# Kernel optimization log

Measured on AMD Instinct MI355X. Metric: run time of the kernel, lower is better.

## Reference

```python
import jax, jax.numpy as jnp
from jax import lax
import numpy as np

T, B, D, H = 4096, 32, 512, 256


def setup_inputs() -> dict:
    key = jax.random.key(0)
    ks = jax.random.split(key, 8)
    s_ih = 1.0 / np.sqrt(H)
    inp = {
        "x": jax.random.normal(ks[0], (T, B, D), dtype=jnp.float32),
        "reset": jax.random.randint(ks[1], (T, B), 0, 2, dtype=jnp.int32),
        # PyTorch nn.LSTM params, gate order (i, f, g, o)
        "W_ih": jax.random.uniform(ks[2], (4 * H, D), jnp.float32, -s_ih, s_ih),
        "W_hh": jax.random.uniform(ks[3], (4 * H, H), jnp.float32, -s_ih, s_ih),
        "b_ih": jax.random.uniform(ks[4], (4 * H,), jnp.float32, -s_ih, s_ih),
        "b_hh": jax.random.uniform(ks[5], (4 * H,), jnp.float32, -s_ih, s_ih),
        "W_proj": jax.random.uniform(ks[6], (1, H), jnp.float32, -s_ih, s_ih),
        "b_proj": jax.random.uniform(ks[7], (1,), jnp.float32, -s_ih, s_ih),
    }
    return inp


def _lstm_with_reset(x, reset, W_ih, W_hh, b_ih, b_hh):
    # Precompute input contribution for all timesteps: [T, B, 4H]
    xW = jnp.einsum("tbd,gd->tbg", x, W_ih) + b_ih + b_hh
    h0 = jnp.zeros((x.shape[1], H), x.dtype)
    c0 = jnp.zeros((x.shape[1], H), x.dtype)

    def step(carry, inp):
        h, c = carry
        xw, r = inp
        keep = (1 - r).astype(h.dtype)[:, None]  # zero state at episode starts
        h = h * keep
        c = c * keep
        gates = xw + h @ W_hh.T  # [B, 4H]
        i, f, g, o = jnp.split(gates, 4, axis=-1)
        c = jax.nn.sigmoid(f) * c + jax.nn.sigmoid(i) * jnp.tanh(g)
        h = jax.nn.sigmoid(o) * jnp.tanh(c)
        return (h, c), h

    (_, _), hs = lax.scan(step, (h0, c0), (xW, reset))
    return hs  # [T, B, H]


def reference(x, reset, W_ih, W_hh, b_ih, b_hh, W_proj, b_proj):
    hs = _lstm_with_reset(x, reset, W_ih, W_hh, b_ih, b_hh)
    return hs @ W_proj.T + b_proj  # [T, B, 1]
```

## Files before the change

### kernel.cpp

```cpp
#include <hip/hip_runtime.h>
#include <cstdint>
#include <cstddef>

#define T_DIM 4096
#define B_DIM 32
#define D_DIM 512
#define H_DIM 256
#define G_DIM 1024
#define HSTR 264
#define XSTR 1036
#define NBUCK 64

typedef _Float16 h8 __attribute__((ext_vector_type(8)));
typedef float f4 __attribute__((ext_vector_type(4)));

__global__ void seg_build_kernel(const int* __restrict__ reset,
                                 unsigned* __restrict__ starts,
                                 unsigned* __restrict__ segcnt) {
  __shared__ unsigned cnts[256];
  __shared__ unsigned offs[256];
  const int b = blockIdx.x;
  const int tid = threadIdx.x;
  const int t0 = tid * 16;
  unsigned c = 0;
  for (int e = 0; e < 16; ++e) {
    int t = t0 + e;
    bool pred = (t == 0) || (reset[t * B_DIM + b] != 0);
    c += pred ? 1u : 0u;
  }
  cnts[tid] = c;
  __syncthreads();
  if (tid == 0) {
    unsigned run = 0;
    for (int i = 0; i < 256; ++i) { unsigned v = cnts[i]; offs[i] = run; run += v; }
    segcnt[b] = run;
  }
  __syncthreads();
  unsigned o = (unsigned)b * 4096u + offs[tid];
  for (int e = 0; e < 16; ++e) {
    int t = t0 + e;
    bool pred = (t == 0) || (reset[t * B_DIM + b] != 0);
    if (pred) { starts[o++] = (unsigned)t; }
  }
}

__global__ void seg_flat_kernel(const unsigned* __restrict__ starts,
                                const unsigned* __restrict__ segcnt,
                                uint2* __restrict__ flat2,
                                unsigned* __restrict__ meta) {
  __shared__ unsigned offs;
  const int b = blockIdx.x;
  const int tid = threadIdx.x;
  if (tid == 0) {
    unsigned o = 0;
    for (int i = 0; i < b; ++i) o += segcnt[i];
    offs = o;
    if (b == 31) meta[1] = o + segcnt[31];
    if (b == 0) meta[0] = 0u;
  }
  __syncthreads();
  const unsigned cnt = segcnt[b];
  const unsigned off = offs;
  for (unsigned s = tid; s < cnt; s += 256) {
    unsigned t0 = starts[b * 4096u + s];
    unsigned t1 = (s + 1 < cnt) ? starts[b * 4096u + s + 1] : 4096u;
    flat2[off + s] = make_uint2(t0 | ((unsigned)b << 16), t1);
  }
}

__global__ void seg_sort_kernel(const uint2* __restrict__ flat2,
                                uint2* __restrict__ flat,
                                const unsigned* __restrict__ meta) {
  __shared__ unsigned lh[NBUCK];
  __shared__ unsigned cur[NBUCK];
  const unsigned nseg = meta[1];
  const int tid = threadIdx.x;
  const int lane = tid & 63;
  if (tid < NBUCK) lh[tid] = 0u;
  __syncthreads();
  for (unsigned base = 0; base < nseg; base += 1024) {
    unsigned i = base + tid;
    bool act = i < nseg;
    unsigned bk = 0u;
    if (act) {
      uint2 e = flat2[i];
      bk = min(e.y - (e.x & 0xFFFFu), (unsigned)NBUCK) - 1u;
    }
    unsigned long long rem = __ballot(act);
    while (rem) {
      int ld = (int)__ffsll((unsigned long long)rem) - 1;
      unsigned lbk = __shfl(bk, ld);
      unsigned long long meq = __ballot(act && bk == lbk);
      if (lane == ld) atomicAdd(&lh[lbk], (unsigned)__popcll(meq));
      rem &= ~meq;
    }
  }
  __syncthreads();
  if (tid == 0) {
    unsigned run = 0;
    for (int k = NBUCK - 1; k >= 0; --k) { cur[k] = run; run += lh[k]; }
  }
  __syncthreads();
  for (unsigned base = 0; base < nseg; base += 1024) {
    unsigned i = base + tid;
    bool act = i < nseg;
    uint2 e = make_uint2(0u, 0u);
    unsigned bk = 0u;
    if (act) {
      e = flat2[i];
      bk = min(e.y - (e.x & 0xFFFFu), (unsigned)NBUCK) - 1u;
    }
    unsigned long long rem = __ballot(act);
    unsigned pos = 0u;
    while (rem) {
      int ld = (int)__ffsll((unsigned long long)rem) - 1;
      unsigned lbk = __shfl(bk, ld);
      unsigned long long meq = __ballot(act && bk == lbk);
      unsigned bs = 0u;
      if (lane == ld) bs = atomicAdd(&cur[lbk], (unsigned)__popcll(meq));
      bs = __shfl(bs, ld);
      if (act && bk == lbk)
        pos = bs + (unsigned)__popcll(meq & ((1ull << lane) - 1ull));
      rem &= ~meq;
    }
    if (act) flat[pos] = e;
  }
}

__global__ void wpack_kernel(const float* __restrict__ Whh,
                             _Float16* __restrict__ wpack) {
  int gid = blockIdx.x * 256 + threadIdx.x;
  int nt = gid >> 9;
  int rem = gid & 511;
  int ks = rem >> 6;
  int l = rem & 63;
  int n = nt * 16 + (l & 15);
  int k = ks * 32 + (l >> 4) * 8;
  const float* src = Whh + (size_t)n * H_DIM + k;
  f4 v0 = *(const f4*)src;
  f4 v1 = *(const f4*)(src + 4);
  h8 wv = {(_Float16)v0.x, (_Float16)v0.y, (_Float16)v0.z, (_Float16)v0.w,
           (_Float16)v1.x, (_Float16)v1.y, (_Float16)v1.z, (_Float16)v1.w};
  *(h8*)(wpack + (size_t)gid * 8) = wv;
}

__global__ __launch_bounds__(256) void xcvt_kernel(const float* __restrict__ X,
                                                   _Float16* __restrict__ xh) {
  const int n8 = (T_DIM * B_DIM * D_DIM) / 8;
  int stride = gridDim.x * blockDim.x;
  for (int i = blockIdx.x * blockDim.x + threadIdx.x; i < n8; i += stride) {
    const float* s = X + (size_t)i * 8;
    f4 a = *(const f4*)s;
    f4 b = *(const f4*)(s + 4);
    h8 v = {(_Float16)a.x, (_Float16)a.y, (_Float16)a.z, (_Float16)a.w,
            (_Float16)b.x, (_Float16)b.y, (_Float16)b.z, (_Float16)b.w};
    *(h8*)(xh + (size_t)i * 8) = v;
  }
}

__global__ void wihpack_kernel(const float* __restrict__ Wih,
                               _Float16* __restrict__ wihp) {
  int gid = blockIdx.x * 256 + threadIdx.x;
  int nt = gid >> 10;
  int ks = (gid >> 6) & 15;
  int l = gid & 63;
  int n = nt * 16 + (l & 15);
  int k = ks * 32 + (l >> 4) * 8;
  const float* src = Wih + (size_t)n * D_DIM + k;
  f4 v0 = *(const f4*)src;
  f4 v1 = *(const f4*)(src + 4);
  h8 wv = {(_Float16)v0.x, (_Float16)v0.y, (_Float16)v0.z, (_Float16)v0.w,
           (_Float16)v1.x, (_Float16)v1.y, (_Float16)v1.z, (_Float16)v1.w};
  *(h8*)(wihp + (size_t)gid * 8) = wv;
}

#define BM 128
#define BN 128
#define BK 32

__global__ __launch_bounds__(256) void xw_gemm_direct(
    const _Float16* __restrict__ xh, const _Float16* __restrict__ wihp,
    const float* __restrict__ bih, const float* __restrict__ bhh,
    _Float16* __restrict__ xw) {
  const int tid = threadIdx.x;
  const int lane = tid & 63;
  const int wave = tid >> 6;
  const unsigned wg = blockIdx.x;
  const unsigned xcd = wg & 7u;
  const unsigned idx = wg >> 3;
  const size_t m0 = (size_t)(xcd * 128u + (idx >> 3)) * BM;
  const int n0 = (int)(idx & 7u) * BN;
  const int wm = (wave & 1) * 64;
  const int wn = (wave >> 1) * 64;
  const int q = lane >> 4;
  const int r = lane & 15;

  f4 acc[4][4];
#pragma unroll
  for (int i = 0; i < 4; ++i)
#pragma unroll
    for (int j = 0; j < 4; ++j) { f4 z = {0.f, 0.f, 0.f, 0.f}; acc[i][j] = z; }

  const _Float16* aBase = xh + (m0 + (size_t)(wm + r)) * D_DIM + q * 8;
  const _Float16* bBase = wihp + ((size_t)(((n0 + wn) >> 4) * 16) * 64 + lane) * 8;

#pragma unroll 4
  for (int ks = 0; ks < 16; ++ks) {
    h8 af[4], bf[4];
#pragma unroll
    for (int mi = 0; mi < 4; ++mi)
      af[mi] = *(const h8*)(aBase + (size_t)mi * (16 * D_DIM) + ks * 32);
#pragma unroll
    for (int ni = 0; ni < 4; ++ni)
      bf[ni] = *(const h8*)(bBase + (size_t)(ni * 16 + ks) * (64 * 8));
#pragma unroll
    for (int mi = 0; mi < 4; ++mi)
#pragma unroll
      for (int ni = 0; ni < 4; ++ni)
        acc[mi][ni] = __builtin_amdgcn_mfma_f32_16x16x32_f16(af[mi], bf[ni], acc[mi][ni], 0, 0, 0);
  }

#pragma unroll
  for (int mi = 0; mi < 4; ++mi) {
#pragma unroll
    for (int ni = 0; ni < 4; ++ni) {
      int n = n0 + wn + ni * 16 + r;
      float bias = bih[n] + bhh[n];
#pragma unroll
      for (int reg = 0; reg < 4; ++reg) {
        size_t m = m0 + (size_t)(wm + mi * 16 + q * 4 + reg);
        xw[m * G_DIM + n] = (_Float16)(acc[mi][ni][reg] + bias);
      }
    }
  }
}

__global__ __launch_bounds__(256) void xw_gemm_kernel(
    const float* __restrict__ X, const float* __restrict__ Wih,
    const float* __restrict__ bih, const float* __restrict__ bhh,
    _Float16* __restrict__ xw) {
  __shared__ _Float16 As[BM * BK];
  __shared__ _Float16 Bs[BN * BK];
  const int tid = threadIdx.x;
  const int lane = tid & 63;
  const int wave = tid >> 6;
  const unsigned wg = blockIdx.x;
  const unsigned xcd = wg & 7u;
  const unsigned idx = wg >> 3;
  const size_t m0 = (size_t)(xcd * 128u + (idx >> 3)) * BM;
  const int n0 = (int)(idx & 7u) * BN;
  const int wm = (wave & 1) * 64;
  const int wn = (wave >> 1) * 64;
  const int q = lane >> 4;
  const int r = lane & 15;

  f4 acc[4][4];
#pragma unroll
  for (int i = 0; i < 4; ++i)
#pragma unroll
    for (int j = 0; j < 4; ++j) { f4 z = {0.f, 0.f, 0.f, 0.f}; acc[i][j] = z; }

  const int srow = tid >> 1;
  const int kh = (tid & 1) * 16;

  for (int k0 = 0; k0 < D_DIM; k0 += BK) {
    const float* ax = X + (m0 + (size_t)srow) * D_DIM + k0 + kh;
    const float* bx = Wih + ((size_t)(n0 + srow)) * D_DIM + k0 + kh;
    f4 a0 = *(const f4*)(ax);
    f4 a1 = *(const f4*)(ax + 4);
    f4 a2 = *(const f4*)(ax + 8);
    f4 a3 = *(const f4*)(ax + 12);
    f4 b0 = *(const f4*)(bx);
    f4 b1 = *(const f4*)(bx + 4);
    f4 b2 = *(const f4*)(bx + 8);
    f4 b3 = *(const f4*)(bx + 12);
    h8 ha0 = {(_Float16)a0.x, (_Float16)a0.y, (_Float16)a0.z, (_Float16)a0.w,
              (_Float16)a1.x, (_Float16)a1.y, (_Float16)a1.z, (_Float16)a1.w};
    h8 ha1 = {(_Float16)a2.x, (_Float16)a2.y, (_Float16)a2.z, (_Float16)a2.w,
              (_Float16)a3.x, (_Float16)a3.y, (_Float16)a3.z, (_Float16)a3.w};
    h8 hb0 = {(_Float16)b0.x, (_Float16)b0.y, (_Float16)b0.z, (_Float16)b0.w,
              (_Float16)b1.x, (_Float16)b1.y, (_Float16)b1.z, (_Float16)b1.w};
    h8 hb1 = {(_Float16)b2.x, (_Float16)b2.y, (_Float16)b2.z, (_Float16)b2.w,
              (_Float16)b3.x, (_Float16)b3.y, (_Float16)b3.z, (_Float16)b3.w};
    *(h8*)(As + srow * BK + kh) = ha0;
    *(h8*)(As + srow * BK + kh + 8) = ha1;
    *(h8*)(Bs + srow * BK + kh) = hb0;
    *(h8*)(Bs + srow * BK + kh + 8) = hb1;
    __syncthreads();

    h8 af[4], bf[4];
#pragma unroll
    for (int mi = 0; mi < 4; ++mi)
      af[mi] = *(const h8*)(As + (wm + mi * 16 + r) * BK + q * 8);
#pragma unroll
    for (int ni = 0; ni < 4; ++ni)
      bf[ni] = *(const h8*)(Bs + (wn + ni * 16 + r) * BK + q * 8);
#pragma unroll
    for (int mi = 0; mi < 4; ++mi)
#pragma unroll
      for (int ni = 0; ni < 4; ++ni)
        acc[mi][ni] = __builtin_amdgcn_mfma_f32_16x16x32_f16(af[mi], bf[ni], acc[mi][ni], 0, 0, 0);
    __syncthreads();
  }

#pragma unroll
  for (int mi = 0; mi < 4; ++mi) {
#pragma unroll
    for (int ni = 0; ni < 4; ++ni) {
      int n = n0 + wn + ni * 16 + r;
      float bias = bih[n] + bhh[n];
#pragma unroll
      for (int reg = 0; reg < 4; ++reg) {
        size_t m = m0 + (size_t)(wm + mi * 16 + q * 4 + reg);
        xw[m * G_DIM + n] = (_Float16)(acc[mi][ni][reg] + bias);
      }
    }
  }
}

__device__ __forceinline__ float sigmf(float x) {
  return __builtin_amdgcn_rcpf(1.f + __expf(-x));
}
__device__ __forceinline__ float tanhf_(float x) {
  return 2.f * __builtin_amdgcn_rcpf(1.f + __expf(-2.f * x)) - 1.f;
}
__device__ __forceinline__ f4 MF(h8 a, h8 b, f4 c) {
  return __builtin_amdgcn_mfma_f32_16x16x32_f16(a, b, c, 0, 0, 0);
}

#define WPKp(g, j, ks) \
  ((const h8*)(wpack + (((size_t)((((g)*16 + 2*w + (j)) * 8 + (ks))) * 64 + l) * 8)))
#define ARD(mt, ks) (*(const h8*)(Hbuf + (16*(mt) + r16) * HSTR + (ks)*32 + q*8))

#define MFK_REG(KS) do {                                                   \
  h8 a0_ = ARD(0, KS), a1_ = ARD(1, KS);                                   \
  _Pragma("unroll") for (int g = 0; g < 4; ++g)                            \
  _Pragma("unroll") for (int j = 0; j < 2; ++j) {                          \
    acc[0][g][j] = MF(a0_, wr[g][j][KS], acc[0][g][j]);                    \
    acc[1][g][j] = MF(a1_, wr[g][j][KS], acc[1][g][j]); }                  \
} while (0)

#define MFK_W2() do {                                                      \
  h8 a0_ = ARD(0, 2), a1_ = ARD(1, 2);                                     \
  _Pragma("unroll") for (int g = 0; g < 4; ++g)                            \
  _Pragma("unroll") for (int j = 0; j < 2; ++j) {                          \
    h8 b_ = *(const h8*)(Wlds + (size_t)((((g)*16 + 2*w + (j)) * 64 + l)) * 8); \
    acc[0][g][j] = MF(a0_, b_, acc[0][g][j]);                              \
    acc[1][g][j] = MF(a1_, b_, acc[1][g][j]); }                            \
} while (0)

#define MFK_S(BUF, KS) do {                                                \
  h8 a0_ = ARD(0, KS), a1_ = ARD(1, KS);                                   \
  _Pragma("unroll") for (int g = 0; g < 4; ++g)                            \
  _Pragma("unroll") for (int j = 0; j < 2; ++j) {                          \
    acc[0][g][j] = MF(a0_, BUF[g][j], acc[0][g][j]);                       \
    acc[1][g][j] = MF(a1_, BUF[g][j], acc[1][g][j]); }                     \
} while (0)

#define LOAD_S(BUF, KS) do {                                               \
  _Pragma("unroll") for (int g = 0; g < 4; ++g)                            \
  _Pragma("unroll") for (int j = 0; j < 2; ++j)                            \
    BUF[g][j] = *WPKp(g, j, KS);                                           \
} while (0)

#define XRD(MT, G, J) do {                                                 \
  f4 xv;                                                                   \
  int rb_ = 16*(MT) + q*4;                                                 \
  int nn_ = (G)*256 + w*32 + 16*(J) + r16;                                 \
  xv.x = (float)xwlds[(rb_+0)*XSTR + nn_];                                 \
  xv.y = (float)xwlds[(rb_+1)*XSTR + nn_];                                 \
  xv.z = (float)xwlds[(rb_+2)*XSTR + nn_];                                 \
  xv.w = (float)xwlds[(rb_+3)*XSTR + nn_];                                 \
  acc[MT][G][J] += xv; } while (0)

#define CONTROL_STEP do {                                                     \
  int m = tid;                                                                \
  bool aliv = alivef[m] != 0;                                                 \
  if (aliv) {                                                                 \
    unsigned oi = outix[m];                                                   \
    if (oi != 0xFFFFFFFFu) {                                                  \
      float s = bp;                                                           \
      _Pragma("unroll") for (int ww = 0; ww < 8; ++ww) s += pbuf[ww][m];      \
      __builtin_nontemporal_store(s, &out[oi]);                               \
    }                                                                         \
  }                                                                           \
  bool cont = aliv && (tcur[m] + 1 < tend[m]);                                \
  bool need = aliv && !cont;                                                  \
  unsigned long long bal = __ballot(need);                                    \
  if (cont) {                                                                 \
    int t = tcur[m] + 1;                                                      \
    tcur[m] = t; keepm[m] = 1.f;                                              \
    unsigned row = (unsigned)t * 32u + (unsigned)bcol[m];                     \
    trowB[m] = row * 2048u; outix[m] = row;                                   \
  }                                                                           \
  if (bal) {                                                                  \
    unsigned cntp = (unsigned)__popcll(bal);                                  \
    int ldr = (int)__ffsll(bal) - 1;                                          \
    unsigned basep = 0;                                                       \
    if ((tid & 63) == ldr) basep = atomicAdd(ctr, cntp);                      \
    basep = __shfl(basep, ldr);                                               \
    if (need) {                                                               \
      unsigned idx = basep +                                                  \
          (unsigned)__popcll(bal & ((1ull << (tid & 63)) - 1ull));            \
      if (idx < nseg) {                                                       \
        uint2 sg = flat[idx];                                                 \
        int t0s = (int)(sg.x & 0xFFFFu); int bb = (int)(sg.x >> 16);          \
        tcur[m] = t0s; tend[m] = (int)sg.y; bcol[m] = bb; keepm[m] = 0.f;     \
        unsigned row = (unsigned)t0s * 32u + (unsigned)bb;                    \
        trowB[m] = row * 2048u; outix[m] = row;                               \
        h8 zz = {0,0,0,0,0,0,0,0};                                            \
        _Pragma("unroll") for (int i2 = 0; i2 < 33; ++i2)                     \
          *(h8*)(Hbuf + (size_t)m * HSTR + i2 * 8) = zz;                      \
      } else {                                                                \
        alivef[m] = 0; outix[m] = 0xFFFFFFFFu; trowB[m] = 0;                  \
        keepm[m] = 0.f;                                                       \
      }                                                                       \
    }                                                                         \
  }                                                                           \
} while (0)

__global__ __attribute__((amdgpu_flat_work_group_size(512, 512),
                          amdgpu_waves_per_eu(2, 2)))
void lstm_scan_mfma(
    const _Float16* __restrict__ xw,
    const _Float16* __restrict__ wpack,
    const float* __restrict__ Wproj,
    const float* __restrict__ bproj,
    const uint2* __restrict__ flat,
    unsigned* __restrict__ meta,
    float* __restrict__ out) {
  __shared__ __align__(16) _Float16 Wlds[64 * 64 * 8];
  __shared__ __align__(16) _Float16 xwlds[32 * XSTR];
  __shared__ __align__(16) _Float16 Hbuf[32 * HSTR];
  __shared__ __align__(16) float pbuf[8][32];
  __shared__ __align__(16) unsigned trowB[32];
  __shared__ __align__(16) float keepm[32];
  __shared__ unsigned outix[32];
  __shared__ int tcur[32], tend[32], bcol[32], alivef[32];

  const int tid = threadIdx.x;
  const int l = tid & 63;
  const int w = tid >> 6;
  const int q = l >> 4;
  const int r16 = l & 15;
  const char* xwc = (const char*)xw;
  unsigned* ctr = meta;
  const unsigned nseg = meta[1];

  for (int it = 0; it < 16; ++it) {
    int idx = it * 512 + tid;
    int nt = idx >> 6;
    int ll = idx & 63;
    *(h8*)(Wlds + (size_t)idx * 8) =
        *(const h8*)(wpack + (((size_t)(nt * 8 + 2)) * 64 + ll) * 8);
  }
  for (int i = tid; i < 32 * HSTR / 8; i += 512) {
    h8 z = {0,0,0,0,0,0,0,0};
    *(h8*)(Hbuf + (size_t)i * 8) = z;
  }
  h8 wr[4][2][2];
#pragma unroll
  for (int g = 0; g < 4; ++g)
#pragma unroll
    for (int j = 0; j < 2; ++j)
#pragma unroll
      for (int ks = 0; ks < 2; ++ks)
        wr[g][j][ks] = *WPKp(g, j, ks);

  const float wpv0 = Wproj[32 * w + r16];
  const float wpv1 = Wproj[32 * w + 16 + r16];
  const float bp = bproj[0];
  if (tid < 32) {
    alivef[tid] = 1; tcur[tid] = 0; tend[tid] = 0; bcol[tid] = 0;
    outix[tid] = 0xFFFFFFFFu; trowB[tid] = 0; keepm[tid] = 0.f;
  }
  float cst[16];
#pragma unroll
  for (int i = 0; i < 16; ++i) cst[i] = 0.f;
  __syncthreads();
  if (tid < 32) CONTROL_STEP;
  int nalive = __syncthreads_count(tid < 32 ? alivef[tid] : 0);

  while (nalive > 0) {
#pragma unroll
    for (int rnd = 0; rnd < 8; ++rnd) {
      int c = rnd * 8 + w;
      unsigned rowB = trowB[c >> 1];
      const char* src = xwc + (size_t)rowB + (size_t)((c & 1) * 1024) + (size_t)l * 16;
      _Float16* dst = xwlds + (size_t)(c >> 1) * XSTR + (c & 1) * 512;
      __builtin_amdgcn_global_load_lds((const uint32_t*)src, (uint32_t*)dst, 16, 0, 2);
    }

    f4 z4 = {0.f, 0.f, 0.f, 0.f};
    f4 acc[2][4][2];
#pragma unroll
    for (int mt = 0; mt < 2; ++mt)
#pragma unroll
      for (int g = 0; g < 4; ++g)
#pragma unroll
        for (int j = 0; j < 2; ++j) acc[mt][g][j] = z4;
    h8 sA[4][2], sB[4][2];

    LOAD_S(sA, 3); LOAD_S(sB, 4);
    MFK_REG(0);
    MFK_REG(1);
    MFK_W2();
    MFK_S(sA, 3); LOAD_S(sA, 5);
    MFK_S(sB, 4); LOAD_S(sB, 6);
    MFK_S(sA, 5); LOAD_S(sA, 7);
    MFK_S(sB, 6);
    MFK_S(sA, 7);

    __syncthreads();

    XRD(0, 0, 0); XRD(0, 0, 1);
    XRD(0, 1, 0); XRD(0, 1, 1);
    XRD(0, 2, 0); XRD(0, 2, 1);
    XRD(0, 3, 0); XRD(0, 3, 1);
    XRD(1, 0, 0); XRD(1, 0, 1);
    XRD(1, 1, 0); XRD(1, 1, 1);
    XRD(1, 2, 0); XRD(1, 2, 1);
    XRD(1, 3, 0); XRD(1, 3, 1);

    f4 kp0 = *(const f4*)&keepm[q * 4];
    f4 kp1 = *(const f4*)&keepm[16 + q * 4];
    float pr[8];
#pragma unroll
    for (int r = 0; r < 4; ++r) {
      {
        float gi = sigmf(acc[0][0][0][r]);
        float gf = sigmf(acc[0][1][0][r]);
        float gg = tanhf_(acc[0][2][0][r]);
        float go = sigmf(acc[0][3][0][r]);
        float cn = gf * (cst[r] * kp0[r]) + gi * gg;
        cst[r] = cn;
        float hv = go * tanhf_(cn);
        Hbuf[(q * 4 + r) * HSTR + 32 * w + r16] = (_Float16)hv;
        pr[r] = hv * wpv0;
      }
      {
        float gi = sigmf(acc[0][0][1][r]);
        float gf = sigmf(acc[0][1][1][r]);
        float gg = tanhf_(acc[0][2][1][r]);
        float go = sigmf(acc[0][3][1][r]);
        float cn = gf * (cst[4 + r] * kp0[r]) + gi * gg;
        cst[4 + r] = cn;
        float hv = go * tanhf_(cn);
        Hbuf[(q * 4 + r) * HSTR + 32 * w + 16 + r16] = (_Float16)hv;
        pr[r] += hv * wpv1;
      }
    }
#pragma unroll
    for (int r = 0; r < 4; ++r) {
      {
        float gi = sigmf(acc[1][0][0][r]);
        float gf = sigmf(acc[1][1][0][r]);
        float gg = tanhf_(acc[1][2][0][r]);
        float go = sigmf(acc[1][3][0][r]);
        float cn = gf * (cst[8 + r] * kp1[r]) + gi * gg;
        cst[8 + r] = cn;
        float hv = go * tanhf_(cn);
        Hbuf[(16 + q * 4 + r) * HSTR + 32 * w + r16] = (_Float16)hv;
        pr[4 + r] = hv * wpv0;
      }
      {
        float gi = sigmf(acc[1][0][1][r]);
        float gf = sigmf(acc[1][1][1][r]);
        float gg = tanhf_(acc[1][2][1][r]);
        float go = sigmf(acc[1][3][1][r]);
        float cn = gf * (cst[12 + r] * kp1[r]) + gi * gg;
        cst[12 + r] = cn;
        float hv = go * tanhf_(cn);
        Hbuf[(16 + q * 4 + r) * HSTR + 32 * w + 16 + r16] = (_Float16)hv;
        pr[4 + r] += hv * wpv1;
      }
    }
#pragma unroll
    for (int jj = 0; jj < 8; ++jj) {
      pr[jj] += __shfl_xor(pr[jj], 1);
      pr[jj] += __shfl_xor(pr[jj], 2);
      pr[jj] += __shfl_xor(pr[jj], 4);
      pr[jj] += __shfl_xor(pr[jj], 8);
    }
    if (r16 == 0) {
#pragma unroll
      for (int jj = 0; jj < 8; ++jj)
        pbuf[w][16 * (jj >> 2) + q * 4 + (jj & 3)] = pr[jj];
    }

    __syncthreads();
    if (tid < 32) CONTROL_STEP;
    nalive = __syncthreads_count(tid < 32 ? alivef[tid] : 0);
  }
}

extern "C" void kernel_launch(void* const* d_in, const int* in_sizes, int n_in,
                              void* d_out, int out_size, void* d_ws, size_t ws_size,
                              hipStream_t stream) {
  const float* x = (const float*)d_in[0];
  const int* reset = (const int*)d_in[1];
  const float* Wih = (const float*)d_in[2];
  const float* Whh = (const float*)d_in[3];
  const float* bih = (const float*)d_in[4];
  const float* bhh = (const float*)d_in[5];
  const float* Wproj = (const float*)d_in[6];
  const float* bproj = (const float*)d_in[7];
  float* out = (float*)d_out;

  char* ws = (char*)d_ws;
  _Float16* xw = (_Float16*)ws;
  unsigned* starts = (unsigned*)(ws + 268435456ULL);
  unsigned* segcnt = (unsigned*)(ws + 268959744ULL);
  uint2* flat = (uint2*)(ws + 268959872ULL);
  _Float16* wpack = (_Float16*)(ws + 270008448ULL);
  unsigned* meta = (unsigned*)(ws + 270532736ULL);
  _Float16* xh = (_Float16*)(ws + 270532864ULL);
  _Float16* wihp = (_Float16*)(ws + 404750592ULL);
  const bool big = ws_size >= 405799168ULL;
  uint2* flat2 = (uint2*)ws;

  hipLaunchKernelGGL(seg_build_kernel, dim3(32), dim3(256), 0, stream,
                     reset, starts, segcnt);
  hipLaunchKernelGGL(seg_flat_kernel, dim3(32), dim3(256), 0, stream,
                     starts, segcnt, flat2, meta);
  hipLaunchKernelGGL(seg_sort_kernel, dim3(1), dim3(1024), 0, stream,
                     flat2, flat, meta);
  hipLaunchKernelGGL(wpack_kernel, dim3(128), dim3(256), 0, stream,
                     Whh, wpack);
  if (big) {
    hipLaunchKernelGGL(xcvt_kernel, dim3(2048), dim3(256), 0, stream, x, xh);
    hipLaunchKernelGGL(wihpack_kernel, dim3(256), dim3(256), 0, stream,
                       Wih, wihp);
    hipLaunchKernelGGL(xw_gemm_direct, dim3(8192), dim3(256), 0, stream,
                       xh, wihp, bih, bhh, xw);
  } else {
    hipLaunchKernelGGL(xw_gemm_kernel, dim3(8192), dim3(256), 0, stream,
                       x, Wih, bih, bhh, xw);
  }
  hipLaunchKernelGGL(lstm_scan_mfma, dim3(256), dim3(512), 0, stream,
                     xw, wpack, Wproj, bproj, flat, meta, out);
}
```

Baseline: 1.318 ms.

## Use LDS-staged f16 GEMM for input projection and 16-wave LSTM scan blocks

Replaces the direct-from-global packed-weight input GEMM with an LDS-staged version. It converts W_ih to plain row-major f16 and fills shared memory with global_load_lds in K=64 chunks. The recurrent scan kernel now runs 1024 threads (16 waves) per block instead of 512, so each wave owns 16 hidden columns rather than 32. This halves per-thread accumulators, register-held W_hh fragments and cell state, aiming to spread the per-step recurrent GEMM and gate math over more waves. The cost is more waves meeting at each per-step barrier, a larger projection reduction, and a global_load_lds cache-policy change.

```diff
diff --git a/kernel.cpp b/kernel.cpp
--- a/kernel.cpp
+++ b/kernel.cpp
@@ -158,38 +158,35 @@
   }
 }
 
-__global__ void wihpack_kernel(const float* __restrict__ Wih,
-                               _Float16* __restrict__ wihp) {
-  int gid = blockIdx.x * 256 + threadIdx.x;
-  int nt = gid >> 10;
-  int ks = (gid >> 6) & 15;
-  int l = gid & 63;
-  int n = nt * 16 + (l & 15);
-  int k = ks * 32 + (l >> 4) * 8;
-  const float* src = Wih + (size_t)n * D_DIM + k;
-  f4 v0 = *(const f4*)src;
-  f4 v1 = *(const f4*)(src + 4);
-  h8 wv = {(_Float16)v0.x, (_Float16)v0.y, (_Float16)v0.z, (_Float16)v0.w,
-           (_Float16)v1.x, (_Float16)v1.y, (_Float16)v1.z, (_Float16)v1.w};
-  *(h8*)(wihp + (size_t)gid * 8) = wv;
-}
-
-#define BM 128
-#define BN 128
-#define BK 32
-
-__global__ __launch_bounds__(256) void xw_gemm_direct(
-    const _Float16* __restrict__ xh, const _Float16* __restrict__ wihp,
+__global__ __launch_bounds__(256) void whcvt_kernel(const float* __restrict__ Wih,
+                                                    _Float16* __restrict__ whp) {
+  int i = blockIdx.x * 256 + threadIdx.x;
+  const float* s = Wih + (size_t)i * 8;
+  f4 a = *(const f4*)s;
+  f4 b = *(const f4*)(s + 4);
+  h8 v = {(_Float16)a.x, (_Float16)a.y, (_Float16)a.z, (_Float16)a.w,
+          (_Float16)b.x, (_Float16)b.y, (_Float16)b.z, (_Float16)b.w};
+  *(h8*)(whp + (size_t)i * 8) = v;
+}
+
+#define GBM 128
+#define GBN 128
+#define GBK 64
+
+__global__ __launch_bounds__(256) void xw_gemm_f16(
+    const _Float16* __restrict__ xh, const _Float16* __restrict__ whp,
     const float* __restrict__ bih, const float* __restrict__ bhh,
     _Float16* __restrict__ xw) {
+  __shared__ __align__(16) _Float16 As[GBM * GBK];
+  __shared__ __align__(16) _Float16 Bs[GBN * GBK];
   const int tid = threadIdx.x;
   const int lane = tid & 63;
   const int wave = tid >> 6;
   const unsigned wg = blockIdx.x;
   const unsigned xcd = wg & 7u;
   const unsigned idx = wg >> 3;
-  const size_t m0 = (size_t)(xcd * 128u + (idx >> 3)) * BM;
-  const int n0 = (int)(idx & 7u) * BN;
+  const size_t m0 = (size_t)(xcd * 128u + (idx >> 3)) * GBM;
+  const int n0 = (int)(idx & 7u) * GBN;
   const int wm = (wave & 1) * 64;
   const int wn = (wave >> 1) * 64;
   const int q = lane >> 4;
@@ -201,23 +198,44 @@
 #pragma unroll
     for (int j = 0; j < 4; ++j) { f4 z = {0.f, 0.f, 0.f, 0.f}; acc[i][j] = z; }
 
-  const _Float16* aBase = xh + (m0 + (size_t)(wm + r)) * D_DIM + q * 8;
-  const _Float16* bBase = wihp + ((size_t)(((n0 + wn) >> 4) * 16) * 64 + lane) * 8;
-
-#pragma unroll 4
-  for (int ks = 0; ks < 16; ++ks) {
-    h8 af[4], bf[4];
+  const char* aSrc = (const char*)xh + m0 * (D_DIM * 2);
+  const char* bSrc = (const char*)whp + (size_t)n0 * (D_DIM * 2);
+
+  for (int k0 = 0; k0 < D_DIM; k0 += GBK) {
+#pragma unroll
+    for (int i = 0; i < 4; ++i) {
+      int o = tid * 16 + i * 4096;
+      int row = o >> 7;
+      int colb = o & 127;
+      __builtin_amdgcn_global_load_lds(
+          (const uint32_t*)(aSrc + (size_t)row * (D_DIM * 2) + k0 * 2 + colb),
+          (uint32_t*)((char*)As + o), 16, 0, 0);
+      __builtin_amdgcn_global_load_lds(
+          (const uint32_t*)(bSrc + (size_t)row * (D_DIM * 2) + k0 * 2 + colb),
+          (uint32_t*)((char*)Bs + o), 16, 0, 0);
+    }
+    __syncthreads();
+
+    h8 af[4][2], bf[4][2];
 #pragma unroll
     for (int mi = 0; mi < 4; ++mi)
-      af[mi] = *(const h8*)(aBase + (size_t)mi * (16 * D_DIM) + ks * 32);
+#pragma unroll
+      for (int ks = 0; ks < 2; ++ks)
+        af[mi][ks] = *(const h8*)(As + (wm + mi * 16 + r) * GBK + ks * 32 + q * 8);
 #pragma unroll
     for (int ni = 0; ni < 4; ++ni)
-      bf[ni] = *(const h8*)(bBase + (size_t)(ni * 16 + ks) * (64 * 8));
-#pragma unroll
-    for (int mi = 0; mi < 4; ++mi)
-#pragma unroll
-      for (int ni = 0; ni < 4; ++ni)
-        acc[mi][ni] = __builtin_amdgcn_mfma_f32_16x16x32_f16(af[mi], bf[ni], acc[mi][ni], 0, 0, 0);
+#pragma unroll
+      for (int ks = 0; ks < 2; ++ks)
+        bf[ni][ks] = *(const h8*)(Bs + (wn + ni * 16 + r) * GBK + ks * 32 + q * 8);
+#pragma unroll
+    for (int ks = 0; ks < 2; ++ks)
+#pragma unroll
+      for (int mi = 0; mi < 4; ++mi)
+#pragma unroll
+        for (int ni = 0; ni < 4; ++ni)
+          acc[mi][ni] = __builtin_amdgcn_mfma_f32_16x16x32_f16(
+              af[mi][ks], bf[ni][ks], acc[mi][ni], 0, 0, 0);
+    __syncthreads();
   }
 
 #pragma unroll
@@ -234,6 +252,10 @@
     }
   }
 }
+
+#define BM 128
+#define BN 128
+#define BK 32
 
 __global__ __launch_bounds__(256) void xw_gemm_kernel(
     const float* __restrict__ X, const float* __restrict__ Wih,
@@ -328,50 +350,46 @@
   return __builtin_amdgcn_mfma_f32_16x16x32_f16(a, b, c, 0, 0, 0);
 }
 
-#define WPKp(g, j, ks) \
-  ((const h8*)(wpack + (((size_t)((((g)*16 + 2*w + (j)) * 8 + (ks))) * 64 + l) * 8)))
+#define WPK16(g, ks) \
+  ((const h8*)(wpack + (((size_t)(((g)*16 + w) * 8 + (ks))) * 64 + l) * 8))
 #define ARD(mt, ks) (*(const h8*)(Hbuf + (16*(mt) + r16) * HSTR + (ks)*32 + q*8))
 
 #define MFK_REG(KS) do {                                                   \
   h8 a0_ = ARD(0, KS), a1_ = ARD(1, KS);                                   \
-  _Pragma("unroll") for (int g = 0; g < 4; ++g)                            \
-  _Pragma("unroll") for (int j = 0; j < 2; ++j) {                          \
-    acc[0][g][j] = MF(a0_, wr[g][j][KS], acc[0][g][j]);                    \
-    acc[1][g][j] = MF(a1_, wr[g][j][KS], acc[1][g][j]); }                  \
+  _Pragma("unroll") for (int g = 0; g < 4; ++g) {                          \
+    acc[0][g] = MF(a0_, wr[g][KS], acc[0][g]);                             \
+    acc[1][g] = MF(a1_, wr[g][KS], acc[1][g]); }                           \
 } while (0)
 
 #define MFK_W2() do {                                                      \
   h8 a0_ = ARD(0, 2), a1_ = ARD(1, 2);                                     \
-  _Pragma("unroll") for (int g = 0; g < 4; ++g)                            \
-  _Pragma("unroll") for (int j = 0; j < 2; ++j) {                          \
-    h8 b_ = *(const h8*)(Wlds + (size_t)((((g)*16 + 2*w + (j)) * 64 + l)) * 8); \
-    acc[0][g][j] = MF(a0_, b_, acc[0][g][j]);                              \
-    acc[1][g][j] = MF(a1_, b_, acc[1][g][j]); }                            \
+  _Pragma("unroll") for (int g = 0; g < 4; ++g) {                          \
+    h8 b_ = *(const h8*)(Wlds + (size_t)((((g)*16 + w) * 64 + l)) * 8);    \
+    acc[0][g] = MF(a0_, b_, acc[0][g]);                                    \
+    acc[1][g] = MF(a1_, b_, acc[1][g]); }                                  \
 } while (0)
 
 #define MFK_S(BUF, KS) do {                                                \
   h8 a0_ = ARD(0, KS), a1_ = ARD(1, KS);                                   \
-  _Pragma("unroll") for (int g = 0; g < 4; ++g)                            \
-  _Pragma("unroll") for (int j = 0; j < 2; ++j) {                          \
-    acc[0][g][j] = MF(a0_, BUF[g][j], acc[0][g][j]);                       \
-    acc[1][g][j] = MF(a1_, BUF[g][j], acc[1][g][j]); }                     \
+  _Pragma("unroll") for (int g = 0; g < 4; ++g) {                          \
+    acc[0][g] = MF(a0_, BUF[g], acc[0][g]);                                \
+    acc[1][g] = MF(a1_, BUF[g], acc[1][g]); }                              \
 } while (0)
 
 #define LOAD_S(BUF, KS) do {                                               \
   _Pragma("unroll") for (int g = 0; g < 4; ++g)                            \
-  _Pragma("unroll") for (int j = 0; j < 2; ++j)                            \
-    BUF[g][j] = *WPKp(g, j, KS);                                           \
+    BUF[g] = *WPK16(g, KS);                                                \
 } while (0)
 
-#define XRD(MT, G, J) do {                                                 \
+#define XRD(MT, G) do {                                                    \
   f4 xv;                                                                   \
   int rb_ = 16*(MT) + q*4;                                                 \
-  int nn_ = (G)*256 + w*32 + 16*(J) + r16;                                 \
+  int nn_ = (G)*256 + hh;                                                  \
   xv.x = (float)xwlds[(rb_+0)*XSTR + nn_];                                 \
   xv.y = (float)xwlds[(rb_+1)*XSTR + nn_];                                 \
   xv.z = (float)xwlds[(rb_+2)*XSTR + nn_];                                 \
   xv.w = (float)xwlds[(rb_+3)*XSTR + nn_];                                 \
-  acc[MT][G][J] += xv; } while (0)
+  acc[MT][G] += xv; } while (0)
 
 #define CONTROL_STEP do {                                                     \
   int m = tid;                                                                \
@@ -380,7 +398,7 @@
     unsigned oi = outix[m];                                                   \
     if (oi != 0xFFFFFFFFu) {                                                  \
       float s = bp;                                                           \
-      _Pragma("unroll") for (int ww = 0; ww < 8; ++ww) s += pbuf[ww][m];      \
+      _Pragma("unroll") for (int ww = 0; ww < 16; ++ww) s += pbuf[ww][m];     \
       __builtin_nontemporal_store(s, &out[oi]);                               \
     }                                                                         \
   }                                                                           \
@@ -419,9 +437,7 @@
   }                                                                           \
 } while (0)
 
-__global__ __attribute__((amdgpu_flat_work_group_size(512, 512),
-                          amdgpu_waves_per_eu(2, 2)))
-void lstm_scan_mfma(
+__global__ __launch_bounds__(1024) void lstm_scan_mfma(
     const _Float16* __restrict__ xw,
     const _Float16* __restrict__ wpack,
     const float* __restrict__ Wproj,
@@ -432,7 +448,7 @@
   __shared__ __align__(16) _Float16 Wlds[64 * 64 * 8];
   __shared__ __align__(16) _Float16 xwlds[32 * XSTR];
   __shared__ __align__(16) _Float16 Hbuf[32 * HSTR];
-  __shared__ __align__(16) float pbuf[8][32];
+  __shared__ __align__(16) float pbuf[16][32];
   __shared__ __align__(16) unsigned trowB[32];
   __shared__ __align__(16) float keepm[32];
   __shared__ unsigned outix[32];
@@ -443,63 +459,57 @@
   const int w = tid >> 6;
   const int q = l >> 4;
   const int r16 = l & 15;
+  const int hh = 16 * w + r16;
   const char* xwc = (const char*)xw;
   unsigned* ctr = meta;
   const unsigned nseg = meta[1];
 
-  for (int it = 0; it < 16; ++it) {
-    int idx = it * 512 + tid;
+  for (int it = 0; it < 4; ++it) {
+    int idx = it * 1024 + tid;
     int nt = idx >> 6;
     int ll = idx & 63;
     *(h8*)(Wlds + (size_t)idx * 8) =
         *(const h8*)(wpack + (((size_t)(nt * 8 + 2)) * 64 + ll) * 8);
   }
-  for (int i = tid; i < 32 * HSTR / 8; i += 512) {
+  for (int i = tid; i < 32 * HSTR / 8; i += 1024) {
     h8 z = {0,0,0,0,0,0,0,0};
     *(h8*)(Hbuf + (size_t)i * 8) = z;
   }
-  h8 wr[4][2][2];
+  h8 wr[4][2];
 #pragma unroll
   for (int g = 0; g < 4; ++g)
 #pragma unroll
-    for (int j = 0; j < 2; ++j)
-#pragma unroll
-      for (int ks = 0; ks < 2; ++ks)
-        wr[g][j][ks] = *WPKp(g, j, ks);
-
-  const float wpv0 = Wproj[32 * w + r16];
-  const float wpv1 = Wproj[32 * w + 16 + r16];
+    for (int ks = 0; ks < 2; ++ks)
+      wr[g][ks] = *WPK16(g, ks);
+
+  const float wpv = Wproj[hh];
   const float bp = bproj[0];
   if (tid < 32) {
     alivef[tid] = 1; tcur[tid] = 0; tend[tid] = 0; bcol[tid] = 0;
     outix[tid] = 0xFFFFFFFFu; trowB[tid] = 0; keepm[tid] = 0.f;
   }
-  float cst[16];
-#pragma unroll
-  for (int i = 0; i < 16; ++i) cst[i] = 0.f;
+  float cst[8] = {0, 0, 0, 0, 0, 0, 0, 0};
   __syncthreads();
   if (tid < 32) CONTROL_STEP;
   int nalive = __syncthreads_count(tid < 32 ? alivef[tid] : 0);
 
   while (nalive > 0) {
 #pragma unroll
-    for (int rnd = 0; rnd < 8; ++rnd) {
-      int c = rnd * 8 + w;
+    for (int rnd = 0; rnd < 4; ++rnd) {
+      int c = rnd * 16 + w;
       unsigned rowB = trowB[c >> 1];
       const char* src = xwc + (size_t)rowB + (size_t)((c & 1) * 1024) + (size_t)l * 16;
       _Float16* dst = xwlds + (size_t)(c >> 1) * XSTR + (c & 1) * 512;
-      __builtin_amdgcn_global_load_lds((const uint32_t*)src, (uint32_t*)dst, 16, 0, 2);
+      __builtin_amdgcn_global_load_lds((const uint32_t*)src, (uint32_t*)dst, 16, 0, 0);
     }
 
     f4 z4 = {0.f, 0.f, 0.f, 0.f};
-    f4 acc[2][4][2];
+    f4 acc[2][4];
 #pragma unroll
     for (int mt = 0; mt < 2; ++mt)
 #pragma unroll
-      for (int g = 0; g < 4; ++g)
-#pragma unroll
-        for (int j = 0; j < 2; ++j) acc[mt][g][j] = z4;
-    h8 sA[4][2], sB[4][2];
+      for (int g = 0; g < 4; ++g) acc[mt][g] = z4;
+    h8 sA[4], sB[4];
 
     LOAD_S(sA, 3); LOAD_S(sB, 4);
     MFK_REG(0);
@@ -513,67 +523,35 @@
 
     __syncthreads();
 
-    XRD(0, 0, 0); XRD(0, 0, 1);
-    XRD(0, 1, 0); XRD(0, 1, 1);
-    XRD(0, 2, 0); XRD(0, 2, 1);
-    XRD(0, 3, 0); XRD(0, 3, 1);
-    XRD(1, 0, 0); XRD(1, 0, 1);
-    XRD(1, 1, 0); XRD(1, 1, 1);
-    XRD(1, 2, 0); XRD(1, 2, 1);
-    XRD(1, 3, 0); XRD(1, 3, 1);
+    XRD(0, 0); XRD(0, 1); XRD(0, 2); XRD(0, 3);
+    XRD(1, 0); XRD(1, 1); XRD(1, 2); XRD(1, 3);
 
     f4 kp0 = *(const f4*)&keepm[q * 4];
     f4 kp1 = *(const f4*)&keepm[16 + q * 4];
     float pr[8];
 #pragma unroll
     for (int r = 0; r < 4; ++r) {
-      {
-        float gi = sigmf(acc[0][0][0][r]);
-        float gf = sigmf(acc[0][1][0][r]);
-        float gg = tanhf_(acc[0][2][0][r]);
-        float go = sigmf(acc[0][3][0][r]);
-        float cn = gf * (cst[r] * kp0[r]) + gi * gg;
-        cst[r] = cn;
-        float hv = go * tanhf_(cn);
-        Hbuf[(q * 4 + r) * HSTR + 32 * w + r16] = (_Float16)hv;
-        pr[r] = hv * wpv0;
-      }
-      {
-        float gi = sigmf(acc[0][0][1][r]);
-        float gf = sigmf(acc[0][1][1][r]);
-        float gg = tanhf_(acc[0][2][1][r]);
-        float go = sigmf(acc[0][3][1][r]);
-        float cn = gf * (cst[4 + r] * kp0[r]) + gi * gg;
-        cst[4 + r] = cn;
-        float hv = go * tanhf_(cn);
-        Hbuf[(q * 4 + r) * HSTR + 32 * w + 16 + r16] = (_Float16)hv;
-        pr[r] += hv * wpv1;
-      }
+      float gi = sigmf(acc[0][0][r]);
+      float gf = sigmf(acc[0][1][r]);
+      float gg = tanhf_(acc[0][2][r]);
+      float go = sigmf(acc[0][3][r]);
+      float cn = gf * (cst[r] * kp0[r]) + gi * gg;
+      cst[r] = cn;
+      float hv = go * tanhf_(cn);
+      Hbuf[(q * 4 + r) * HSTR + hh] = (_Float16)hv;
+      pr[r] = hv * wpv;
     }
 #pragma unroll
     for (int r = 0; r < 4; ++r) {
-      {
-        float gi = sigmf(acc[1][0][0][r]);
-        float gf = sigmf(acc[1][1][0][r]);
-        float gg = tanhf_(acc[1][2][0][r]);
-        float go = sigmf(acc[1][3][0][r]);
-        float cn = gf * (cst[8 + r] * kp1[r]) + gi * gg;
-        cst[8 + r] = cn;
-        float hv = go * tanhf_(cn);
-        Hbuf[(16 + q * 4 + r) * HSTR + 32 * w + r16] = (_Float16)hv;
-        pr[4 + r] = hv * wpv0;
-      }
-      {
-        float gi = sigmf(acc[1][0][1][r]);
-        float gf = sigmf(acc[1][1][1][r]);
-        float gg = tanhf_(acc[1][2][1][r]);
-        float go = sigmf(acc[1][3][1][r]);
-        float cn = gf * (cst[12 + r] * kp1[r]) + gi * gg;
-        cst[12 + r] = cn;
-        float hv = go * tanhf_(cn);
-        Hbuf[(16 + q * 4 + r) * HSTR + 32 * w + 16 + r16] = (_Float16)hv;
-        pr[4 + r] += hv * wpv1;
-      }
+      float gi = sigmf(acc[1][0][r]);
+      float gf = sigmf(acc[1][1][r]);
+      float gg = tanhf_(acc[1][2][r]);
+      float go = sigmf(acc[1][3][r]);
+      float cn = gf * (cst[4 + r] * kp1[r]) + gi * gg;
+      cst[4 + r] = cn;
+      float hv = go * tanhf_(cn);
+      Hbuf[(16 + q * 4 + r) * HSTR + hh] = (_Float16)hv;
+      pr[4 + r] = hv * wpv;
     }
 #pragma unroll
     for (int jj = 0; jj < 8; ++jj) {
@@ -615,7 +593,7 @@
   _Float16* wpack = (_Float16*)(ws + 270008448ULL);
   unsigned* meta = (unsigned*)(ws + 270532736ULL);
   _Float16* xh = (_Float16*)(ws + 270532864ULL);
-  _Float16* wihp = (_Float16*)(ws + 404750592ULL);
+  _Float16* whp = (_Float16*)(ws + 404750592ULL);
   const bool big = ws_size >= 405799168ULL;
   uint2* flat2 = (uint2*)ws;
 
@@ -629,14 +607,14 @@
                      Whh, wpack);
   if (big) {
     hipLaunchKernelGGL(xcvt_kernel, dim3(2048), dim3(256), 0, stream, x, xh);
-    hipLaunchKernelGGL(wihpack_kernel, dim3(256), dim3(256), 0, stream,
-                       Wih, wihp);
-    hipLaunchKernelGGL(xw_gemm_direct, dim3(8192), dim3(256), 0, stream,
-                       xh, wihp, bih, bhh, xw);
+    hipLaunchKernelGGL(whcvt_kernel, dim3(256), dim3(256), 0, stream,
+                       Wih, whp);
+    hipLaunchKernelGGL(xw_gemm_f16, dim3(8192), dim3(256), 0, stream,
+                       xh, whp, bih, bhh, xw);
   } else {
     hipLaunchKernelGGL(xw_gemm_kernel, dim3(8192), dim3(256), 0, stream,
                        x, Wih, bih, bhh, xw);
   }
-  hipLaunchKernelGGL(lstm_scan_mfma, dim3(256), dim3(512), 0, stream,
+  hipLaunchKernelGGL(lstm_scan_mfma, dim3(256), dim3(1024), 0, stream,
                      xw, wpack, Wproj, bproj, flat, meta, out);
 }
```

Result: faster. 1.168 ms (-11.3%).
